# Performance work log

Measured on AMD Instinct MI355X. Metric: run time of the kernel, lower is better.

Reference implementation:

```python
import jax, jax.numpy as jnp
import numpy as np

B, N, F, O = 4, 4096, 64, 64


def setup_inputs() -> dict:
    key = jax.random.key(0)
    k0, k1, k2, k3, k4 = jax.random.split(key, 5)
    x = jax.random.normal(k0, (B, N, F), dtype=jnp.float32)
    # adj_transform: Linear(2F -> 1): weight (2F,), bias scalar
    adj_w = jax.random.normal(k1, (2 * F,), dtype=jnp.float32) * (1.0 / np.sqrt(2 * F))
    adj_b = jax.random.normal(k2, (), dtype=jnp.float32)
    # GCN weight: xavier_normal_ over (F, O)
    weight = jax.random.normal(k3, (F, O), dtype=jnp.float32) * np.sqrt(2.0 / (F + O))
    bias = jax.random.normal(k4, (O,), dtype=jnp.float32)
    return {"x": x, "adj_w": adj_w, "adj_b": adj_b, "weight": weight, "bias": bias}


def reference(x, adj_w, adj_b, weight, bias):
    f = x.shape[-1]
    # Original: tmp[b,i,j] = x[b,j]; adj[b,i,j] = Linear(cat(x[b,j], x[b,i]))
    # = x[b,j]\u00b7adj_w[:F] + x[b,i]\u00b7adj_w[F:] + adj_b  (exact decomposition,
    # avoids materializing the (B,N,N,2F) concat tensor)
    s_col = jnp.einsum('bnf,f->bn', x, adj_w[:f])   # contributes along j
    s_row = jnp.einsum('bnf,f->bn', x, adj_w[f:])   # contributes along i
    adj = s_row[:, :, None] + s_col[:, None, :] + adj_b  # (B, N, N)
    # symmetric degree normalization with clamp(min=1)
    deg_inv_sqrt = jnp.clip(adj.sum(axis=-1), 1.0, None) ** -0.5  # (B, N)
    adj = deg_inv_sqrt[:, :, None] * adj * deg_inv_sqrt[:, None, :]
    out = jnp.einsum('bij,bjo->bio', adj, x @ weight) + bias
    return jax.nn.relu(out)
```

## Files before the change

kernel.cpp:

```cpp
#include <hip/hip_runtime.h>

#define Bq 4
#define Nq 4096
#define Fq 64
#define Oq 64


__global__ __launch_bounds__(256) void k1_rowdots(
    const float* __restrict__ x, const float* __restrict__ adj_w,
    float* __restrict__ s_row, float* __restrict__ s_col,
    float* __restrict__ scol_sum) {
  int r = blockIdx.x * 256 + threadIdx.x;
  const float4* xr = reinterpret_cast<const float4*>(x + (size_t)r * Fq);
  const float4* w0 = reinterpret_cast<const float4*>(adj_w);
  const float4* w1 = reinterpret_cast<const float4*>(adj_w + Fq);
  float sc = 0.f, sr = 0.f;
#pragma unroll
  for (int k = 0; k < Fq / 4; ++k) {
    float4 v = xr[k];
    float4 a = w0[k];
    float4 b = w1[k];
    sc += v.x * a.x + v.y * a.y + v.z * a.z + v.w * a.w;
    sr += v.x * b.x + v.y * b.y + v.z * b.z + v.w * b.w;
  }
  s_col[r] = sc;
  s_row[r] = sr;
  __shared__ float red[256];
  red[threadIdx.x] = sc;
  __syncthreads();
  for (int s = 128; s > 0; s >>= 1) {
    if (threadIdx.x < s) red[threadIdx.x] += red[threadIdx.x + s];
    __syncthreads();
  }
  if (threadIdx.x == 0) {
    int b = r >> 12;
    atomicAdd(&scol_sum[b], red[0]);
  }
}

__global__ __launch_bounds__(256) void k2_weighted(
    const float* __restrict__ x, const float* __restrict__ s_row,
    const float* __restrict__ s_col, const float* __restrict__ scol_sum,
    const float* __restrict__ adj_bp, float* __restrict__ xd,
    float* __restrict__ xsd) {
  int b = blockIdx.x >> 5;
  int chunk = blockIdx.x & 31;
  int f = threadIdx.x & 63;
  int jsub = threadIdx.x >> 6;
  const float adj_b = adj_bp[0];
  const float scs = scol_sum[b];
  const int jcnt = Nq / 32;
  int j0 = chunk * jcnt;
  float axd = 0.f, axsd = 0.f;
  for (int j = j0 + jsub; j < j0 + jcnt; j += 4) {
    int row = b * Nq + j;
    float srj = s_row[row];
    float scj = s_col[row];
    float rowsum = fmaf((float)Nq, srj + adj_b, scs);
    float dj = rsqrtf(fmaxf(rowsum, 1.0f));
    float xv = x[(size_t)row * Fq + f];
    axd = fmaf(dj, xv, axd);
    axsd = fmaf(scj * dj, xv, axsd);
  }
  __shared__ float red[2][4][64];
  red[0][jsub][f] = axd;
  red[1][jsub][f] = axsd;
  __syncthreads();
  if (threadIdx.x < 64) {
    float t0 = red[0][0][f] + red[0][1][f] + red[0][2][f] + red[0][3][f];
    atomicAdd(&xd[b * Fq + f], t0);
  } else if (threadIdx.x < 128) {
    float t1 = red[1][0][f] + red[1][1][f] + red[1][2][f] + red[1][3][f];
    atomicAdd(&xsd[b * Fq + f], t1);
  }
}

__global__ __launch_bounds__(256) void k3_out(
    const float* __restrict__ s_row, const float* __restrict__ scol_sum,
    const float* __restrict__ adj_bp, const float* __restrict__ xd,
    const float* __restrict__ xsd, const float* __restrict__ weight,
    const float* __restrict__ bias, float* __restrict__ out) {
  int bx = blockIdx.x;
  int b = bx >> 8;
  int ibase = (bx & 255) << 4;
  const float adj_b = adj_bp[0];
  const float scs = scol_sum[b];
  __shared__ float u[64], v[64];
  int t = threadIdx.x;
  if (t < 128) {
    int o = t & 63;
    const float* src = (t < 64) ? (xd + b * Fq) : (xsd + b * Fq);
    float acc = 0.f;
#pragma unroll
    for (int f = 0; f < Fq; ++f) acc = fmaf(src[f], weight[f * Oq + o], acc);
    if (t < 64)
      u[o] = acc;
    else
      v[o] = acc;
  }
  __syncthreads();
  int row = ibase + (t >> 4);
  int rglob = b * Nq + row;
  int o0 = (t & 15) * 4;
  float sr = s_row[rglob];
  float rowsum = fmaf((float)Nq, sr + adj_b, scs);
  float di = rsqrtf(fmaxf(rowsum, 1.0f));
  float a = di * (sr + adj_b);
  float4 r;
  r.x = fmaxf(0.f, fmaf(a, u[o0 + 0], fmaf(di, v[o0 + 0], bias[o0 + 0])));
  r.y = fmaxf(0.f, fmaf(a, u[o0 + 1], fmaf(di, v[o0 + 1], bias[o0 + 1])));
  r.z = fmaxf(0.f, fmaf(a, u[o0 + 2], fmaf(di, v[o0 + 2], bias[o0 + 2])));
  r.w = fmaxf(0.f, fmaf(a, u[o0 + 3], fmaf(di, v[o0 + 3], bias[o0 + 3])));
  reinterpret_cast<float4*>(out + (size_t)rglob * Oq)[t & 15] = r;
}

extern "C" void kernel_launch(void* const* d_in, const int* in_sizes, int n_in,
                              void* d_out, int out_size, void* d_ws,
                              size_t ws_size, hipStream_t stream) {
  const float* x = (const float*)d_in[0];
  const float* adj_w = (const float*)d_in[1];
  const float* adj_b = (const float*)d_in[2];
  const float* weight = (const float*)d_in[3];
  const float* bias = (const float*)d_in[4];
  float* out = (float*)d_out;

  float* ws = (float*)d_ws;
  float* s_row = ws;
  float* s_col = ws + Bq * Nq;
  float* scol_sum = ws + 2 * Bq * Nq;
  float* xd = scol_sum + Bq;
  float* xsd = xd + Bq * Fq;

  hipMemsetAsync(scol_sum, 0, (Bq + 2 * Bq * Fq) * sizeof(float), stream);

  k1_rowdots<<<(Bq * Nq) / 256, 256, 0, stream>>>(x, adj_w, s_row, s_col,
                                                  scol_sum);
  k2_weighted<<<Bq * 32, 256, 0, stream>>>(x, s_row, s_col, scol_sum, adj_b,
                                           xd, xsd);
  k3_out<<<(Bq * Nq) / 16, 256, 0, stream>>>(s_row, scol_sum, adj_b, xd, xsd,
                                             weight, bias, out);
}
```

Baseline: 80.73 us.

## Replace atomics and memset with deterministic per-block partials; enlarge k3 row tiles

Each block now writes its partial sums (column-score sums and the weighted x reductions) to a dedicated slot instead of using atomicAdd. Consumer kernels reduce those partials themselves, which removes the hipMemsetAsync call and its separate launch. k3 now processes 64 rows per block over four passes, so the per-block recomputation of u and v happens 256 times instead of 1024. The cost is redundant partial reductions in every consumer block and fewer blocks in k3.

```diff
diff --git a/kernel.cpp b/kernel.cpp
--- a/kernel.cpp
+++ b/kernel.cpp
@@ -9,7 +9,7 @@
 __global__ __launch_bounds__(256) void k1_rowdots(
     const float* __restrict__ x, const float* __restrict__ adj_w,
     float* __restrict__ s_row, float* __restrict__ s_col,
-    float* __restrict__ scol_sum) {
+    float* __restrict__ blocksum) {
   int r = blockIdx.x * 256 + threadIdx.x;
   const float4* xr = reinterpret_cast<const float4*>(x + (size_t)r * Fq);
   const float4* w0 = reinterpret_cast<const float4*>(adj_w);
@@ -32,23 +32,22 @@
     if (threadIdx.x < s) red[threadIdx.x] += red[threadIdx.x + s];
     __syncthreads();
   }
-  if (threadIdx.x == 0) {
-    int b = r >> 12;
-    atomicAdd(&scol_sum[b], red[0]);
-  }
+  if (threadIdx.x == 0) blocksum[blockIdx.x] = red[0];
 }
 
 __global__ __launch_bounds__(256) void k2_weighted(
     const float* __restrict__ x, const float* __restrict__ s_row,
-    const float* __restrict__ s_col, const float* __restrict__ scol_sum,
-    const float* __restrict__ adj_bp, float* __restrict__ xd,
-    float* __restrict__ xsd) {
+    const float* __restrict__ s_col, const float* __restrict__ blocksum,
+    const float* __restrict__ adj_bp, float* __restrict__ pxd,
+    float* __restrict__ pxsd) {
   int b = blockIdx.x >> 5;
   int chunk = blockIdx.x & 31;
   int f = threadIdx.x & 63;
   int jsub = threadIdx.x >> 6;
   const float adj_b = adj_bp[0];
-  const float scs = scol_sum[b];
+  float scs = 0.f;
+#pragma unroll
+  for (int k = 0; k < 16; ++k) scs += blocksum[b * 16 + k];
   const int jcnt = Nq / 32;
   int j0 = chunk * jcnt;
   float axd = 0.f, axsd = 0.f;
@@ -67,29 +66,42 @@
   red[1][jsub][f] = axsd;
   __syncthreads();
   if (threadIdx.x < 64) {
-    float t0 = red[0][0][f] + red[0][1][f] + red[0][2][f] + red[0][3][f];
-    atomicAdd(&xd[b * Fq + f], t0);
+    pxd[blockIdx.x * 64 + f] =
+        red[0][0][f] + red[0][1][f] + red[0][2][f] + red[0][3][f];
   } else if (threadIdx.x < 128) {
-    float t1 = red[1][0][f] + red[1][1][f] + red[1][2][f] + red[1][3][f];
-    atomicAdd(&xsd[b * Fq + f], t1);
+    pxsd[blockIdx.x * 64 + f] =
+        red[1][0][f] + red[1][1][f] + red[1][2][f] + red[1][3][f];
   }
 }
 
 __global__ __launch_bounds__(256) void k3_out(
-    const float* __restrict__ s_row, const float* __restrict__ scol_sum,
-    const float* __restrict__ adj_bp, const float* __restrict__ xd,
-    const float* __restrict__ xsd, const float* __restrict__ weight,
+    const float* __restrict__ s_row, const float* __restrict__ blocksum,
+    const float* __restrict__ adj_bp, const float* __restrict__ pxd,
+    const float* __restrict__ pxsd, const float* __restrict__ weight,
     const float* __restrict__ bias, float* __restrict__ out) {
-  int bx = blockIdx.x;
-  int b = bx >> 8;
-  int ibase = (bx & 255) << 4;
+  int b = blockIdx.x >> 6;
+  int ibase = (blockIdx.x & 63) << 6;
   const float adj_b = adj_bp[0];
-  const float scs = scol_sum[b];
-  __shared__ float u[64], v[64];
+  float scs = 0.f;
+#pragma unroll
+  for (int k = 0; k < 16; ++k) scs += blocksum[b * 16 + k];
+  __shared__ float xdl[64], xsdl[64], u[64], v[64];
   int t = threadIdx.x;
   if (t < 128) {
+    int f = t & 63;
+    const float* p = ((t < 64) ? pxd : pxsd) + (size_t)(b * 32) * 64 + f;
+    float a = 0.f;
+#pragma unroll
+    for (int c = 0; c < 32; ++c) a += p[c * 64];
+    if (t < 64)
+      xdl[f] = a;
+    else
+      xsdl[f] = a;
+  }
+  __syncthreads();
+  if (t < 128) {
     int o = t & 63;
-    const float* src = (t < 64) ? (xd + b * Fq) : (xsd + b * Fq);
+    const float* src = (t < 64) ? xdl : xsdl;
     float acc = 0.f;
 #pragma unroll
     for (int f = 0; f < Fq; ++f) acc = fmaf(src[f], weight[f * Oq + o], acc);
@@ -99,19 +111,22 @@
       v[o] = acc;
   }
   __syncthreads();
-  int row = ibase + (t >> 4);
-  int rglob = b * Nq + row;
   int o0 = (t & 15) * 4;
-  float sr = s_row[rglob];
-  float rowsum = fmaf((float)Nq, sr + adj_b, scs);
-  float di = rsqrtf(fmaxf(rowsum, 1.0f));
-  float a = di * (sr + adj_b);
-  float4 r;
-  r.x = fmaxf(0.f, fmaf(a, u[o0 + 0], fmaf(di, v[o0 + 0], bias[o0 + 0])));
-  r.y = fmaxf(0.f, fmaf(a, u[o0 + 1], fmaf(di, v[o0 + 1], bias[o0 + 1])));
-  r.z = fmaxf(0.f, fmaf(a, u[o0 + 2], fmaf(di, v[o0 + 2], bias[o0 + 2])));
-  r.w = fmaxf(0.f, fmaf(a, u[o0 + 3], fmaf(di, v[o0 + 3], bias[o0 + 3])));
-  reinterpret_cast<float4*>(out + (size_t)rglob * Oq)[t & 15] = r;
+#pragma unroll
+  for (int pass = 0; pass < 4; ++pass) {
+    int row = ibase + pass * 16 + (t >> 4);
+    int rg = b * Nq + row;
+    float sr = s_row[rg];
+    float rowsum = fmaf((float)Nq, sr + adj_b, scs);
+    float di = rsqrtf(fmaxf(rowsum, 1.0f));
+    float a = di * (sr + adj_b);
+    float4 r;
+    r.x = fmaxf(0.f, fmaf(a, u[o0 + 0], fmaf(di, v[o0 + 0], bias[o0 + 0])));
+    r.y = fmaxf(0.f, fmaf(a, u[o0 + 1], fmaf(di, v[o0 + 1], bias[o0 + 1])));
+    r.z = fmaxf(0.f, fmaf(a, u[o0 + 2], fmaf(di, v[o0 + 2], bias[o0 + 2])));
+    r.w = fmaxf(0.f, fmaf(a, u[o0 + 3], fmaf(di, v[o0 + 3], bias[o0 + 3])));
+    reinterpret_cast<float4*>(out + (size_t)rg * Oq)[t & 15] = r;
+  }
 }
 
 extern "C" void kernel_launch(void* const* d_in, const int* in_sizes, int n_in,
@@ -127,16 +142,13 @@
   float* ws = (float*)d_ws;
   float* s_row = ws;
   float* s_col = ws + Bq * Nq;
-  float* scol_sum = ws + 2 * Bq * Nq;
-  float* xd = scol_sum + Bq;
-  float* xsd = xd + Bq * Fq;
+  float* blocksum = ws + 2 * Bq * Nq;
+  float* pxd = blocksum + 64;
+  float* pxsd = pxd + 128 * 64;
 
-  hipMemsetAsync(scol_sum, 0, (Bq + 2 * Bq * Fq) * sizeof(float), stream);
-
-  k1_rowdots<<<(Bq * Nq) / 256, 256, 0, stream>>>(x, adj_w, s_row, s_col,
-                                                  scol_sum);
-  k2_weighted<<<Bq * 32, 256, 0, stream>>>(x, s_row, s_col, scol_sum, adj_b,
-                                           xd, xsd);
-  k3_out<<<(Bq * Nq) / 16, 256, 0, stream>>>(s_row, scol_sum, adj_b, xd, xsd,
-                                             weight, bias, out);
+  k1_rowdots<<<64, 256, 0, stream>>>(x, adj_w, s_row, s_col, blocksum);
+  k2_weighted<<<Bq * 32, 256, 0, stream>>>(x, s_row, s_col, blocksum, adj_b,
+                                           pxd, pxsd);
+  k3_out<<<256, 256, 0, stream>>>(s_row, blocksum, adj_b, pxd, pxsd, weight,
+                                  bias, out);
 }
```

Result: faster. 78.12 us (-3.2%).
